# Kernel optimization log

Hardware: AMD Instinct MI355X
Metric: run time of the kernel (lower is better)

Reference implementation:

```python
import jax, jax.numpy as jnp
import numpy as np
from math import ceil

N = 20000   # nodes
E = 320000  # edges
D = 128     # num_features == num_hidden
K = ceil(N * 0.1)  # 2000 PMA seeds


def _gcn(x, W, b, src, dst):
    # PyG GCNConv: add self-loops, symmetric deg^-1/2 normalization, sum-aggregate, bias
    n = x.shape[0]
    sl = jnp.arange(n)
    s = jnp.concatenate([src, sl])
    d = jnp.concatenate([dst, sl])
    deg = jax.ops.segment_sum(jnp.ones((s.shape[0],), x.dtype), d, num_segments=n)
    dinv = jax.lax.rsqrt(jnp.maximum(deg, 1e-12))
    norm = dinv[s] * dinv[d]
    h = x @ W
    return jax.ops.segment_sum(h[s] * norm[:, None], d, num_segments=n) + b


def _ln(x, g, b):
    m = jnp.mean(x, -1, keepdims=True)
    v = jnp.var(x, -1, keepdims=True)
    return (x - m) * jax.lax.rsqrt(v + 1e-5) * g + b


def setup_inputs() -> dict:
    key = jax.random.key(0)
    ks = jax.random.split(key, 32)
    w = lambda i, shape: jax.random.normal(ks[i], shape, jnp.float32) * 0.05
    z = lambda shape: jnp.zeros(shape, jnp.float32)
    o = lambda shape: jnp.ones(shape, jnp.float32)
    return {
        "x": jax.random.normal(ks[0], (N, D), jnp.float32),
        "edge_index": jax.random.randint(ks[1], (2, E), 0, N),
        "batch": jnp.zeros((N,), jnp.int32),
        "W1": w(2, (D, D)), "b1": z((D,)),
        "W2": w(3, (D, D)), "b2": z((D,)),
        "S": w(4, (1, K, D)),
        "Wq": w(5, (D, D)), "bq": z((D,)),
        "Wk": w(6, (D, D)), "bk": z((D,)),
        "Wv": w(7, (D, D)), "bv": z((D,)),
        "Wo": w(8, (D, D)), "bo": z((D,)),
        "g0": o((D,)), "be0": z((D,)),
        "g1": o((D,)), "be1": z((D,)),
        "Wl": w(9, (D, D)), "bl": z((D,)),
        "W3": w(10, (D, D)), "b3": z((D,)),
        "W4": w(11, (D, D)), "b4": z((D,)),
        "W5": w(12, (D, D)), "b5": z((D,)),
    }


def reference(x, edge_index, batch, W1, b1, W2, b2, S, Wq, bq, Wk, bk, Wv, bv,
              Wo, bo, g0, be0, g1, be1, Wl, bl, W3, b3, W4, b4, W5, b5):
    src, dst = edge_index[0], edge_index[1]
    h = jax.nn.relu(_gcn(x, W1, b1, src, dst))
    h = jax.nn.relu(_gcn(h, W2, b2, src, dst))
    # B=1 dense batch: mask all-true -> additive attention mask is 0
    Q = S @ Wq + bq                        # [1,K,D]
    Kd = _gcn(h, Wk, bk, src, dst)[None]   # [1,N,D]  (mab_conv='GCN')
    Vd = _gcn(h, Wv, bv, src, dst)[None]   # [1,N,D]
    score = jnp.einsum('bkd,bnd->bkn', Q, Kd) / jnp.sqrt(jnp.float32(D))
    A = jax.nn.softmax(score, axis=1)      # cluster=True: softmax over seed dim
    out = Q + jnp.einsum('bkn,bnd->bkd', A, Vd)
    out = _ln(out, g0, be0)
    out = out + jax.nn.relu(out @ Wo + bo)
    out = _ln(out, g1, be1)
    xl = out @ Wl + bl                     # [1,K,D]
    x_out = jnp.einsum('bkn,bkd->bnd', A, xl)[0]  # attn^T @ x -> [N,D], mask all-true
    h = jax.nn.relu(_gcn(x_out, W3, b3, src, dst))
    h = jax.nn.relu(_gcn(h, W4, b4, src, dst))
    return _gcn(h, W5, b5, src, dst)       # [N,D]
```

## Files before the change

### kernel.cpp

```cpp
#include <hip/hip_runtime.h>

#define NN 20000
#define EE 320000
#define KK 2000
#define KP 2048
#define SCALE 0.08838834764831845f
#define ZSPLIT 16
#define ACHUNKS 625

typedef const float* cfp;
typedef __attribute__((ext_vector_type(8))) short sh8;
typedef __attribute__((ext_vector_type(4))) float f32x4;

static __device__ __forceinline__ float4 ld4(const float* p){ return *reinterpret_cast<const float4*>(p); }
static __device__ __forceinline__ void st4(float* p, float4 v){ *reinterpret_cast<float4*>(p) = v; }

static __device__ __forceinline__ unsigned short f2bf(float f){
    unsigned int u = __float_as_uint(f);
    u = (u + 0x7FFFu + ((u >> 16) & 1u)) >> 16;
    return (unsigned short)u;
}
static __device__ __forceinline__ float bf2f(unsigned short h){
    return __uint_as_float(((unsigned int)h) << 16);
}
static __device__ __forceinline__ sh8 lds8(const unsigned short* p){ return *reinterpret_cast<const sh8*>(p); }

__global__ __launch_bounds__(256) void k_count(const int* dst, int* deg){
    int i = blockIdx.x*256 + threadIdx.x;
    if (i < EE) atomicAdd(&deg[dst[i]], 1);
}

__global__ __launch_bounds__(256) void k_dinv(const int* deg, float* dinv){
    int n = blockIdx.x*256 + threadIdx.x;
    if (n < NN) dinv[n] = rsqrtf((float)deg[n] + 1.0f);
}

__global__ __launch_bounds__(1024) void k_scan(const int* cnt, int* rows){
    __shared__ int part[1024];
    int t = threadIdx.x;
    int base = t*20;
    int s = 0;
    for (int i = 0; i < 20; ++i){ int idx = base+i; if (idx < NN) s += cnt[idx]; }
    part[t] = s; __syncthreads();
    for (int off = 1; off < 1024; off <<= 1){
        int v = (t >= off) ? part[t-off] : 0;
        __syncthreads();
        part[t] += v;
        __syncthreads();
    }
    int run = part[t] - s;
    for (int i = 0; i < 20; ++i){
        int idx = base+i;
        if (idx < NN){ rows[idx] = run; run += cnt[idx]; }
    }
    if (t == 0) rows[NN] = EE;
}

__global__ __launch_bounds__(256) void k_fill(const int* src, const int* dst, const int* rows,
                                              int* cursor, int* col){
    int i = blockIdx.x*256 + threadIdx.x;
    if (i < EE){
        int d = dst[i];
        int pos = rows[d] + atomicAdd(&cursor[d], 1);
        col[pos] = src[i];
    }
}

__global__ __launch_bounds__(256) void conv_wT(cfp w0, cfp w1, cfp w2, cfp w3, cfp w4, cfp w5, cfp w6,
                                               unsigned short* wts){
    const float* in;
    switch (blockIdx.z){
        case 0: in = w0; break; case 1: in = w1; break; case 2: in = w2; break;
        case 3: in = w3; break; case 4: in = w4; break; case 5: in = w5; break;
        default: in = w6; break;
    }
    unsigned short* out = wts + (size_t)blockIdx.z*16384;
    __shared__ float t[64][65];
    int r0 = blockIdx.x*64, c0 = blockIdx.y*64;
    int tid = threadIdx.x;
    for (int i = tid; i < 64*16; i += 256){
        int r = i >> 4, c4 = (i & 15) * 4;
        float4 v = ld4(in + (size_t)(r0+r)*128 + c0 + c4);
        t[r][c4+0]=v.x; t[r][c4+1]=v.y; t[r][c4+2]=v.z; t[r][c4+3]=v.w;
    }
    __syncthreads();
    for (int i = tid; i < 64*16; i += 256){
        int c = i >> 4, r4 = (i & 15) * 4;
        ushort4 o;
        o.x = f2bf(t[r4+0][c]); o.y = f2bf(t[r4+1][c]);
        o.z = f2bf(t[r4+2][c]); o.w = f2bf(t[r4+3][c]);
        *reinterpret_cast<ushort4*>(out + (size_t)(c0+c)*128 + r0 + r4) = o;
    }
}

__global__ __launch_bounds__(512) void gemm128(const float* __restrict__ A, const float* __restrict__ Wm,
                                               float* __restrict__ C, int M,
                                               const float* bias, const float* resid, int relu){
    __shared__ __align__(16) float Ws[128*132];
    __shared__ float As[64*129];
    int tid = threadIdx.x;
    int r0 = blockIdx.x*64;
    for (int i = tid; i < 128*32; i += 512){
        int r = i >> 5, c4 = (i & 31) * 4;
        float4 v = ld4(Wm + r*128 + c4);
        st4(&Ws[r*132 + c4], v);
    }
    for (int i = tid; i < 64*32; i += 512){
        int r = i >> 5, c4 = (i & 31) * 4;
        float4 v = (r0 + r < M) ? ld4(A + (size_t)(r0+r)*128 + c4) : make_float4(0,0,0,0);
        As[r*129 + c4+0] = v.x; As[r*129 + c4+1] = v.y;
        As[r*129 + c4+2] = v.z; As[r*129 + c4+3] = v.w;
    }
    __syncthreads();
    int a = tid >> 5;
    int b = tid & 31;
    float acc[4][4] = {};
    #pragma unroll 4
    for (int d = 0; d < 128; ++d){
        float4 w = ld4(&Ws[d*132 + 4*b]);
        float wv[4] = {w.x, w.y, w.z, w.w};
        float av[4];
        #pragma unroll
        for (int i = 0; i < 4; ++i) av[i] = As[(4*a+i)*129 + d];
        #pragma unroll
        for (int i = 0; i < 4; ++i)
            #pragma unroll
            for (int j = 0; j < 4; ++j)
                acc[i][j] += av[i]*wv[j];
    }
    int cc = 4*b;
    #pragma unroll
    for (int i = 0; i < 4; ++i){
        int r = r0 + 4*a + i;
        if (r < M){
            float v[4];
            #pragma unroll
            for (int j = 0; j < 4; ++j) v[j] = acc[i][j];
            if (bias){
                #pragma unroll
                for (int j = 0; j < 4; ++j) v[j] += bias[cc+j];
            }
            if (relu){
                #pragma unroll
                for (int j = 0; j < 4; ++j) v[j] = fmaxf(v[j], 0.f);
            }
            if (resid){
                float4 rv = ld4(resid + (size_t)r*128 + cc);
                v[0]+=rv.x; v[1]+=rv.y; v[2]+=rv.z; v[3]+=rv.w;
            }
            st4(C + (size_t)r*128 + cc, make_float4(v[0],v[1],v[2],v[3]));
        }
    }
}

__global__ __launch_bounds__(256) void tgemm(const unsigned short* __restrict__ A, int M,
                                             const unsigned short* __restrict__ Wt,
                                             const float* __restrict__ rscale,
                                             unsigned short* __restrict__ C){
    int tid = threadIdx.x;
    int wave = tid >> 6, lane = tid & 63;
    int wm = wave >> 1, wn = wave & 1;
    int m_base = blockIdx.x*64 + wm*32;
    int n_base = blockIdx.y*64 + wn*32;
    int l15 = lane & 15;
    int roff = (lane >> 4) * 8;
    const unsigned short* ap0 = A + (size_t)(m_base + l15)*128 + roff;
    const unsigned short* ap1 = ap0 + 16*128;
    const unsigned short* b0p = Wt + (size_t)(n_base + l15)*128 + roff;
    const unsigned short* b1p = b0p + 16*128;
    f32x4 acc00 = (f32x4)0.f, acc01 = (f32x4)0.f, acc10 = (f32x4)0.f, acc11 = (f32x4)0.f;
    #pragma unroll
    for (int r = 0; r < 128; r += 32){
        sh8 a0 = lds8(ap0 + r);
        sh8 a1 = lds8(ap1 + r);
        sh8 b0 = lds8(b0p + r);
        sh8 b1 = lds8(b1p + r);
        acc00 = __builtin_amdgcn_mfma_f32_16x16x32_bf16(a0, b0, acc00, 0, 0, 0);
        acc01 = __builtin_amdgcn_mfma_f32_16x16x32_bf16(a0, b1, acc01, 0, 0, 0);
        acc10 = __builtin_amdgcn_mfma_f32_16x16x32_bf16(a1, b0, acc10, 0, 0, 0);
        acc11 = __builtin_amdgcn_mfma_f32_16x16x32_bf16(a1, b1, acc11, 0, 0, 0);
    }
    int rq = (lane >> 4) * 4;
    f32x4 accs[2][2] = {{acc00, acc01},{acc10, acc11}};
    #pragma unroll
    for (int mi = 0; mi < 2; ++mi){
        #pragma unroll
        for (int ni = 0; ni < 2; ++ni){
            f32x4 a = accs[mi][ni];
            int gn = n_base + ni*16 + l15;
            #pragma unroll
            for (int reg = 0; reg < 4; ++reg){
                int gm = m_base + mi*16 + rq + reg;
                if (gm < M) C[(size_t)gm*128 + gn] = f2bf(a[reg] * (rscale ? rscale[gm] : 1.f));
            }
        }
    }
}

__global__ __launch_bounds__(256) void gcn_agg_bf(const unsigned short* __restrict__ y, const float* __restrict__ dinv,
                                                  const int* __restrict__ rows, const int* __restrict__ col,
                                                  const float* __restrict__ bias, void* __restrict__ outv,
                                                  int relu, int out_fp32){
    int wid = (int)((blockIdx.x*256 + threadIdx.x) >> 6);
    int lane = threadIdx.x & 63;
    if (wid >= NN) return;
    int f = lane*2;
    ushort2 u = *reinterpret_cast<const ushort2*>(y + (size_t)wid*128 + f);
    float ax = bf2f(u.x), ay = bf2f(u.y);
    int s = rows[wid], e = rows[wid+1];
    int j = s;
    int e8 = s + ((e - s) & ~7);
    for (; j < e8; j += 8){
        ushort2 v[8];
        #pragma unroll
        for (int q = 0; q < 8; ++q){
            int c = col[j+q];
            v[q] = *reinterpret_cast<const ushort2*>(y + (size_t)c*128 + f);
        }
        #pragma unroll
        for (int q = 0; q < 8; ++q){ ax += bf2f(v[q].x); ay += bf2f(v[q].y); }
    }
    for (; j < e; ++j){
        int c0 = col[j];
        ushort2 v0 = *reinterpret_cast<const ushort2*>(y + (size_t)c0*128 + f);
        ax += bf2f(v0.x); ay += bf2f(v0.y);
    }
    float dn = dinv[wid];
    float ox = ax*dn + bias[f];
    float oy = ay*dn + bias[f+1];
    if (relu){ ox = fmaxf(ox, 0.f); oy = fmaxf(oy, 0.f); }
    if (out_fp32){
        *reinterpret_cast<float2*>((float*)outv + (size_t)wid*128 + f) = make_float2(ox, oy);
    } else {
        ushort2 o; o.x = f2bf(ox); o.y = f2bf(oy);
        *reinterpret_cast<ushort2*>((unsigned short*)outv + (size_t)wid*128 + f) = o;
    }
}

__global__ __launch_bounds__(256) void conv_bf16(const float* __restrict__ in, unsigned short* __restrict__ out, int n4){
    int i = blockIdx.x*256 + threadIdx.x;
    if (i < n4){
        float4 v = ld4(in + (size_t)i*4);
        ushort4 o;
        o.x = f2bf(v.x); o.y = f2bf(v.y); o.z = f2bf(v.z); o.w = f2bf(v.w);
        *reinterpret_cast<ushort4*>(out + (size_t)i*4) = o;
    }
}

__global__ __launch_bounds__(256) void conv_bf16_T(const float* __restrict__ in, unsigned short* __restrict__ out,
                                                   int M, int ldout, const float* __restrict__ rscale){
    __shared__ float t[64][65];
    int r0 = blockIdx.x*64, c0 = blockIdx.y*64;
    int tid = threadIdx.x;
    for (int i = tid; i < 64*16; i += 256){
        int r = i >> 4, c4 = (i & 15) * 4;
        float4 v = (r0 + r < M) ? ld4(in + (size_t)(r0+r)*128 + c0 + c4) : make_float4(0,0,0,0);
        if (rscale && r0 + r < M){
            float sc = rscale[r0 + r];
            v.x *= sc; v.y *= sc; v.z *= sc; v.w *= sc;
        }
        t[r][c4+0]=v.x; t[r][c4+1]=v.y; t[r][c4+2]=v.z; t[r][c4+3]=v.w;
    }
    __syncthreads();
    for (int i = tid; i < 64*16; i += 256){
        int c = i >> 4, r4 = (i & 15) * 4;
        if (r0 + r4 < M){
            ushort4 o;
            o.x = f2bf(t[r4+0][c]); o.y = f2bf(t[r4+1][c]);
            o.z = f2bf(t[r4+2][c]); o.w = f2bf(t[r4+3][c]);
            *reinterpret_cast<ushort4*>(out + (size_t)(c0+c)*ldout + r0 + r4) = o;
        }
    }
}

__global__ __launch_bounds__(256) void k_rcp32(const float* __restrict__ zp, const float* __restrict__ dinv,
                                               float* __restrict__ zinv, float* __restrict__ zdinv){
    int n = blockIdx.x*256 + threadIdx.x;
    if (n < NN){
        float s = 0.f;
        #pragma unroll
        for (int y = 0; y < 32; ++y) s += zp[(size_t)y*NN + n];
        float zi = 1.f / s;
        zinv[n] = zi;
        zdinv[n] = zi * dinv[n];
    }
}

__global__ __launch_bounds__(256) void s_gemm_exp(const unsigned short* __restrict__ Kb,
                                                  const unsigned short* __restrict__ Qb2,
                                                  unsigned short* __restrict__ E, float* __restrict__ zpart){
    __shared__ unsigned short Es[64*68];
    int tid = threadIdx.x;
    int wave = tid >> 6, lane = tid & 63;
    int wm = wave >> 1, wn = wave & 1;
    int n_blk = blockIdx.x*64, k_blk = blockIdx.y*64;
    int l15 = lane & 15;
    int roff = (lane >> 4) * 8;
    const unsigned short* ap0 = Kb + (size_t)(n_blk + wm*32 + l15)*128 + roff;
    const unsigned short* ap1 = ap0 + 16*128;
    const unsigned short* bp0 = Qb2 + (size_t)(k_blk + wn*32 + l15)*128 + roff;
    const unsigned short* bp1 = bp0 + 16*128;
    f32x4 acc00 = (f32x4)0.f, acc01 = (f32x4)0.f, acc10 = (f32x4)0.f, acc11 = (f32x4)0.f;
    #pragma unroll
    for (int r = 0; r < 128; r += 32){
        sh8 a0 = lds8(ap0 + r);
        sh8 a1 = lds8(ap1 + r);
        sh8 b0 = lds8(bp0 + r);
        sh8 b1 = lds8(bp1 + r);
        acc00 = __builtin_amdgcn_mfma_f32_16x16x32_bf16(a0, b0, acc00, 0, 0, 0);
        acc01 = __builtin_amdgcn_mfma_f32_16x16x32_bf16(a0, b1, acc01, 0, 0, 0);
        acc10 = __builtin_amdgcn_mfma_f32_16x16x32_bf16(a1, b0, acc10, 0, 0, 0);
        acc11 = __builtin_amdgcn_mfma_f32_16x16x32_bf16(a1, b1, acc11, 0, 0, 0);
    }
    int rq = (lane >> 4) * 4;
    f32x4 accs[2][2] = {{acc00, acc01},{acc10, acc11}};
    #pragma unroll
    for (int mi = 0; mi < 2; ++mi){
        #pragma unroll
        for (int ni = 0; ni < 2; ++ni){
            f32x4 a = accs[mi][ni];
            int c_loc = wn*32 + ni*16 + l15;
            bool kv = (k_blk + c_loc) < KK;
            #pragma unroll
            for (int reg = 0; reg < 4; ++reg){
                int r_loc = wm*32 + mi*16 + rq + reg;
                float e = kv ? __expf(a[reg]*SCALE) : 0.f;
                Es[r_loc*68 + c_loc] = f2bf(e);
            }
        }
    }
    __syncthreads();
    if (tid < 64){
        int n = n_blk + tid;
        if (n < NN){
            float s = 0.f;
            #pragma unroll 8
            for (int j = 0; j < 64; ++j) s += bf2f(Es[tid*68 + j]);
            zpart[(size_t)blockIdx.y*NN + n] = s;
        }
    }
    for (int i = tid; i < 512; i += 256){
        int r = i >> 3, c8 = (i & 7) * 8;
        if (n_blk + r < NN){
            ushort4 lo = *reinterpret_cast<const ushort4*>(&Es[r*68 + c8]);
            ushort4 hi = *reinterpret_cast<const ushort4*>(&Es[r*68 + c8 + 4]);
            unsigned short* dst = E + (size_t)(n_blk + r)*KP + k_blk + c8;
            *reinterpret_cast<ushort4*>(dst) = lo;
            *reinterpret_cast<ushort4*>(dst + 4) = hi;
        }
    }
}

__global__ __launch_bounds__(256) void attn_gemm(const unsigned short* __restrict__ E,
                                                 const unsigned short* __restrict__ Vt,
                                                 float* __restrict__ part){
    __shared__ unsigned short As[64*36];
    int tid = threadIdx.x;
    int wave = tid >> 6, lane = tid & 63;
    int kk0 = blockIdx.x*64;
    int per = (ACHUNKS + ZSPLIT - 1) / ZSPLIT;
    int c0 = blockIdx.y*per;
    int c1 = min(ACHUNKS, c0 + per);
    int l15 = lane & 15;
    int q8 = (lane >> 4) * 8;
    int d0 = wave*32;
    int n_l = tid & 31;
    int k8 = (tid >> 5) * 8;
    f32x4 acc[4][2];
    #pragma unroll
    for (int g = 0; g < 4; ++g){ acc[g][0] = (f32x4)0.f; acc[g][1] = (f32x4)0.f; }
    const unsigned short* ebase = E + (size_t)n_l*KP + kk0 + k8;
    const unsigned short* vb0p = Vt + (size_t)(d0 + l15)*NN + q8;
    const unsigned short* vb1p = vb0p + (size_t)16*NN;
    sh8 etmp = lds8(ebase + (size_t)c0*32*KP);
    sh8 vb0 = lds8(vb0p + c0*32);
    sh8 vb1 = lds8(vb1p + c0*32);
    for (int ch = c0; ch < c1; ++ch){
        unsigned short tmp[8];
        *reinterpret_cast<sh8*>(tmp) = etmp;
        #pragma unroll
        for (int j = 0; j < 8; ++j) As[(k8 + j)*36 + n_l] = tmp[j];
        __syncthreads();
        sh8 etn = (sh8)0, vbn0 = (sh8)0, vbn1 = (sh8)0;
        if (ch + 1 < c1){
            etn  = lds8(ebase + (size_t)(ch+1)*32*KP);
            vbn0 = lds8(vb0p + (ch+1)*32);
            vbn1 = lds8(vb1p + (ch+1)*32);
        }
        #pragma unroll
        for (int g = 0; g < 4; ++g){
            const unsigned short* ap = &As[(g*16 + l15)*36 + q8];
            union { struct { ushort4 lo, hi; } u; sh8 v; } af;
            af.u.lo = *reinterpret_cast<const ushort4*>(ap);
            af.u.hi = *reinterpret_cast<const ushort4*>(ap + 4);
            acc[g][0] = __builtin_amdgcn_mfma_f32_16x16x32_bf16(af.v, vb0, acc[g][0], 0, 0, 0);
            acc[g][1] = __builtin_amdgcn_mfma_f32_16x16x32_bf16(af.v, vb1, acc[g][1], 0, 0, 0);
        }
        __syncthreads();
        etmp = etn; vb0 = vbn0; vb1 = vbn1;
    }
    float* pbase = part + (size_t)blockIdx.y*KK*128;
    int rq = (lane >> 4) * 4;
    #pragma unroll
    for (int g = 0; g < 4; ++g){
        #pragma unroll
        for (int ni = 0; ni < 2; ++ni){
            int d = d0 + ni*16 + l15;
            #pragma unroll
            for (int reg = 0; reg < 4; ++reg){
                int kk = kk0 + g*16 + rq + reg;
                if (kk < KK) pbase[(size_t)kk*128 + d] = acc[g][ni][reg];
            }
        }
    }
}

__global__ __launch_bounds__(256) void xout_gemm(const unsigned short* __restrict__ E,
                                                 const unsigned short* __restrict__ B,
                                                 float* __restrict__ xpart){
    int tid = threadIdx.x;
    int wave = tid >> 6, lane = tid & 63;
    int wm = wave >> 1, wn = wave & 1;
    int m_base = blockIdx.x*64 + wm*32;
    int n_base = blockIdx.y*64 + wn*32;
    int kz = blockIdx.z*1024;
    int l15 = lane & 15;
    int roff = (lane >> 4) * 8;
    const unsigned short* ap0 = E + (size_t)(m_base + l15)*KP + kz + roff;
    const unsigned short* ap1 = ap0 + (size_t)16*KP;
    const unsigned short* bp0 = B + (size_t)(n_base + l15)*KP + kz + roff;
    const unsigned short* bp1 = bp0 + (size_t)16*KP;
    f32x4 acc00 = (f32x4)0.f, acc01 = (f32x4)0.f, acc10 = (f32x4)0.f, acc11 = (f32x4)0.f;
    sh8 a0 = lds8(ap0),      a1 = lds8(ap1),      a2 = lds8(ap0 + 32), a3 = lds8(ap1 + 32);
    sh8 b0 = lds8(bp0),      b1 = lds8(bp1),      b2 = lds8(bp0 + 32), b3 = lds8(bp1 + 32);
    for (int r = 0; r < 1024; r += 64){
        int rn = r + 64;
        sh8 na0 = (sh8)0, na1 = (sh8)0, na2 = (sh8)0, na3 = (sh8)0;
        sh8 nb0 = (sh8)0, nb1 = (sh8)0, nb2 = (sh8)0, nb3 = (sh8)0;
        if (rn < 1024){
            na0 = lds8(ap0 + rn);      na1 = lds8(ap1 + rn);
            na2 = lds8(ap0 + rn + 32); na3 = lds8(ap1 + rn + 32);
            nb0 = lds8(bp0 + rn);      nb1 = lds8(bp1 + rn);
            nb2 = lds8(bp0 + rn + 32); nb3 = lds8(bp1 + rn + 32);
        }
        acc00 = __builtin_amdgcn_mfma_f32_16x16x32_bf16(a0, b0, acc00, 0, 0, 0);
        acc01 = __builtin_amdgcn_mfma_f32_16x16x32_bf16(a0, b1, acc01, 0, 0, 0);
        acc10 = __builtin_amdgcn_mfma_f32_16x16x32_bf16(a1, b0, acc10, 0, 0, 0);
        acc11 = __builtin_amdgcn_mfma_f32_16x16x32_bf16(a1, b1, acc11, 0, 0, 0);
        acc00 = __builtin_amdgcn_mfma_f32_16x16x32_bf16(a2, b2, acc00, 0, 0, 0);
        acc01 = __builtin_amdgcn_mfma_f32_16x16x32_bf16(a2, b3, acc01, 0, 0, 0);
        acc10 = __builtin_amdgcn_mfma_f32_16x16x32_bf16(a3, b2, acc10, 0, 0, 0);
        acc11 = __builtin_amdgcn_mfma_f32_16x16x32_bf16(a3, b3, acc11, 0, 0, 0);
        a0 = na0; a1 = na1; a2 = na2; a3 = na3;
        b0 = nb0; b1 = nb1; b2 = nb2; b3 = nb3;
    }
    float* pbase = xpart + (size_t)blockIdx.z*NN*128;
    int rq = (lane >> 4) * 4;
    f32x4 accs[2][2] = {{acc00, acc01},{acc10, acc11}};
    #pragma unroll
    for (int mi = 0; mi < 2; ++mi){
        #pragma unroll
        for (int ni = 0; ni < 2; ++ni){
            f32x4 a = accs[mi][ni];
            int gn = n_base + ni*16 + l15;
            #pragma unroll
            for (int reg = 0; reg < 4; ++reg){
                int gm = m_base + mi*16 + rq + reg;
                if (gm < NN) pbase[(size_t)gm*128 + gn] = a[reg];
            }
        }
    }
}

__global__ __launch_bounds__(256) void xred(const float* __restrict__ xp, const float* __restrict__ zdinv,
                                            unsigned short* __restrict__ out){
    int i = blockIdx.x*256 + threadIdx.x;
    if (i < NN*32){
        int row = i >> 5;
        float4 p0 = ld4(xp + (size_t)i*4);
        float4 p1 = ld4(xp + (size_t)NN*128 + (size_t)i*4);
        float sc = zdinv[row];
        ushort4 o;
        o.x = f2bf((p0.x + p1.x)*sc);
        o.y = f2bf((p0.y + p1.y)*sc);
        o.z = f2bf((p0.z + p1.z)*sc);
        o.w = f2bf((p0.w + p1.w)*sc);
        *reinterpret_cast<ushort4*>(out + (size_t)i*4) = o;
    }
}

__global__ __launch_bounds__(128) void ln_ker(const float* __restrict__ in, int nparts,
                                              const float* __restrict__ resid,
                                              const float* __restrict__ g, const float* __restrict__ be,
                                              float* __restrict__ out){
    __shared__ float rs[128], rq[128];
    int r = blockIdx.x, t = threadIdx.x;
    float v = 0.f;
    for (int p = 0; p < nparts; ++p) v += in[(size_t)p*KK*128 + r*128 + t];
    if (resid) v += resid[r*128 + t];
    rs[t] = v; rq[t] = v*v;
    __syncthreads();
    for (int off = 64; off > 0; off >>= 1){
        if (t < off){ rs[t] += rs[t+off]; rq[t] += rq[t+off]; }
        __syncthreads();
    }
    float mean = rs[0]*(1.f/128.f);
    float var = rq[0]*(1.f/128.f) - mean*mean;
    out[r*128 + t] = (v - mean)*rsqrtf(var + 1e-5f)*g[t] + be[t];
}

extern "C" void kernel_launch(void* const* d_in, const int* in_sizes, int n_in,
                              void* d_out, int out_size, void* d_ws, size_t ws_size,
                              hipStream_t stream){
    cfp x  = (cfp)d_in[0];
    const int* ei = (const int*)d_in[1];
    const int* esrc = ei;
    const int* edst = ei + EE;
    cfp W1=(cfp)d_in[3], b1=(cfp)d_in[4], W2=(cfp)d_in[5], b2=(cfp)d_in[6];
    cfp S =(cfp)d_in[7];
    cfp Wq=(cfp)d_in[8],  bq=(cfp)d_in[9],  Wk=(cfp)d_in[10], bk=(cfp)d_in[11];
    cfp Wv=(cfp)d_in[12], bv=(cfp)d_in[13], Wo=(cfp)d_in[14], bo=(cfp)d_in[15];
    cfp g0=(cfp)d_in[16], be0=(cfp)d_in[17], g1=(cfp)d_in[18], be1=(cfp)d_in[19];
    cfp Wl=(cfp)d_in[20], bl=(cfp)d_in[21], W3=(cfp)d_in[22], b3=(cfp)d_in[23];
    cfp W4=(cfp)d_in[24], b4=(cfp)d_in[25], W5=(cfp)d_in[26], b5=(cfp)d_in[27];

    char* wsb = (char*)d_ws;
    const size_t MB = 1048576;
    int*   deg    = (int*)  (wsb + 0);
    float* dinv   = (float*)(wsb + 81920);
    int*   rows   = (int*)  (wsb + 163840);
    int*   cursor = (int*)  (wsb + 245760);
    int*   col    = (int*)  (wsb + 327680);
    float* Qb     = (float*)(wsb + 2*MB);
    float* o1     = (float*)(wsb + 3*MB);
    float* o2     = (float*)(wsb + 4*MB);
    float* o3     = (float*)(wsb + 5*MB);
    float* xlb    = (float*)(wsb + 6*MB);
    float* zpart  = (float*)(wsb + 7*MB);
    float* zinv   = (float*)(wsb + 10*MB);
    float* zdinv  = (float*)(wsb + 10*MB + 131072);
    unsigned short* Wts  = (unsigned short*)(wsb + 10*MB + 262144);
    unsigned short* Qbf  = (unsigned short*)(wsb + 11*MB);
    unsigned short* xlt3 = (unsigned short*)(wsb + 11*MB + 524288);
    unsigned short* xbf = (unsigned short*)(wsb + 12*MB);
    unsigned short* h1  = (unsigned short*)(wsb + 17*MB);
    unsigned short* h2  = (unsigned short*)(wsb + 22*MB);
    unsigned short* ybuf= (unsigned short*)(wsb + 27*MB);
    unsigned short* Kbf = (unsigned short*)(wsb + 32*MB);
    unsigned short* Vtz = (unsigned short*)(wsb + 37*MB);
    float* NB3    = (float*)(wsb + 42*MB);
    float* part   = (float*)(wsb + 42*MB);
    float* xpart  = (float*)(wsb + 42*MB);
    unsigned short* E = (unsigned short*)(wsb + 62*MB);
    float* outp   = (float*)d_out;
    unsigned short* h3 = xbf;
    unsigned short* h4 = h1;

    (void)hipMemsetAsync(deg, 0, NN*sizeof(int), stream);
    (void)hipMemsetAsync(cursor, 0, NN*sizeof(int), stream);
    (void)hipMemsetAsync(xlt3, 0, 128*KP*sizeof(unsigned short), stream);

    k_count<<<1250, 256, 0, stream>>>(edst, deg);
    k_dinv<<<79, 256, 0, stream>>>(deg, dinv);
    k_scan<<<1, 1024, 0, stream>>>(deg, rows);
    k_fill<<<1250, 256, 0, stream>>>(esrc, edst, rows, cursor, col);

    conv_wT<<<dim3(2,2,7), 256, 0, stream>>>(W1, W2, Wk, Wv, W3, W4, W5, Wts);
    conv_bf16<<<2500, 256, 0, stream>>>(x, xbf, NN*32);
    unsigned short* W1t = Wts;
    unsigned short* W2t = Wts + 16384;
    unsigned short* Wkt = Wts + 2*16384;
    unsigned short* Wvt = Wts + 3*16384;
    unsigned short* W4t = Wts + 5*16384;
    unsigned short* W5t = Wts + 6*16384;

    const int GN = 313;
    const int GK = 32;

    tgemm<<<dim3(GN,2), 256, 0, stream>>>(xbf, NN, W1t, dinv, ybuf);
    gcn_agg_bf<<<5000, 256, 0, stream>>>(ybuf, dinv, rows, col, b1, h1, 1, 0);
    tgemm<<<dim3(GN,2), 256, 0, stream>>>(h1, NN, W2t, dinv, ybuf);
    gcn_agg_bf<<<5000, 256, 0, stream>>>(ybuf, dinv, rows, col, b2, h2, 1, 0);
    tgemm<<<dim3(GN,2), 256, 0, stream>>>(h2, NN, Wkt, dinv, ybuf);
    gcn_agg_bf<<<5000, 256, 0, stream>>>(ybuf, dinv, rows, col, bk, Kbf, 0, 0);
    gemm128<<<GK, 512, 0, stream>>>(S, Wq, Qb, KK, bq, nullptr, 0);
    conv_bf16<<<250, 256, 0, stream>>>(Qb, Qbf, KK*32);
    s_gemm_exp<<<dim3(GN, GK), 256, 0, stream>>>(Kbf, Qbf, E, zpart);
    k_rcp32<<<79, 256, 0, stream>>>(zpart, dinv, zinv, zdinv);
    tgemm<<<dim3(GN,2), 256, 0, stream>>>(h2, NN, Wvt, dinv, ybuf);
    gcn_agg_bf<<<5000, 256, 0, stream>>>(ybuf, dinv, rows, col, bv, NB3, 0, 1);
    conv_bf16_T<<<dim3(GN, 2), 256, 0, stream>>>(NB3, Vtz, NN, NN, zinv);
    attn_gemm<<<dim3(GK, ZSPLIT), 256, 0, stream>>>(E, Vtz, part);
    ln_ker<<<KK, 128, 0, stream>>>(part, ZSPLIT, Qb, g0, be0, o1);
    gemm128<<<GK, 512, 0, stream>>>(o1, Wo, o2, KK, bo, o1, 1);
    ln_ker<<<KK, 128, 0, stream>>>(o2, 1, nullptr, g1, be1, o3);
    gemm128<<<GK, 512, 0, stream>>>(o3, Wl, xlb, KK, bl, nullptr, 0);
    gemm128<<<GK, 512, 0, stream>>>(xlb, W3, o1, KK, nullptr, nullptr, 0);
    conv_bf16_T<<<dim3(GK, 2), 256, 0, stream>>>(o1, xlt3, KK, KP, nullptr);
    xout_gemm<<<dim3(GN, 2, 2), 256, 0, stream>>>(E, xlt3, xpart);
    xred<<<2500, 256, 0, stream>>>(xpart, zdinv, ybuf);
    gcn_agg_bf<<<5000, 256, 0, stream>>>(ybuf, dinv, rows, col, b3, h3, 1, 0);
    tgemm<<<dim3(GN,2), 256, 0, stream>>>(h3, NN, W4t, dinv, ybuf);
    gcn_agg_bf<<<5000, 256, 0, stream>>>(ybuf, dinv, rows, col, b4, h4, 1, 0);
    tgemm<<<dim3(GN,2), 256, 0, stream>>>(h4, NN, W5t, dinv, ybuf);
    gcn_agg_bf<<<5000, 256, 0, stream>>>(ybuf, dinv, rows, col, b5, outp, 0, 1);
}
```

Measured before the change: 637.4 us.

## Reuse K tiles across seed blocks in score-exp and widen xout tile to full D

s_gemm_exp now has each block keep its 64-row K tile in registers and loop over 8 seed sub-blocks of 64, prefetching the next Q tile. The row sums are accumulated in fp32 registers and reduced with shuffles rather than summed back from the bf16 values in shared memory. The grid drops from 32 to 4 seed chunks, and k_rcp32 sums 4 partials instead of 32. xout_gemm now computes all 128 output columns per block with 8 accumulators per wave, so each block reads its E rows once instead of twice. The cost is fewer blocks, more registers and extra barriers per block.

```diff
diff --git a/kernel.cpp b/kernel.cpp
--- a/kernel.cpp
+++ b/kernel.cpp
@@ -7,6 +7,7 @@
 #define SCALE 0.08838834764831845f
 #define ZSPLIT 16
 #define ACHUNKS 625
+#define ZCH 4
 
 typedef const float* cfp;
 typedef __attribute__((ext_vector_type(8))) short sh8;
@@ -279,7 +280,7 @@
     if (n < NN){
         float s = 0.f;
         #pragma unroll
-        for (int y = 0; y < 32; ++y) s += zp[(size_t)y*NN + n];
+        for (int y = 0; y < ZCH; ++y) s += zp[(size_t)y*NN + n];
         float zi = 1.f / s;
         zinv[n] = zi;
         zdinv[n] = zi * dinv[n];
@@ -290,64 +291,99 @@
                                                   const unsigned short* __restrict__ Qb2,
                                                   unsigned short* __restrict__ E, float* __restrict__ zpart){
     __shared__ unsigned short Es[64*68];
+    __shared__ float zsh[2][64];
     int tid = threadIdx.x;
     int wave = tid >> 6, lane = tid & 63;
     int wm = wave >> 1, wn = wave & 1;
-    int n_blk = blockIdx.x*64, k_blk = blockIdx.y*64;
+    int n_blk = blockIdx.x*64;
+    int k_base = blockIdx.y*512;
     int l15 = lane & 15;
     int roff = (lane >> 4) * 8;
+    int rq = (lane >> 4) * 4;
     const unsigned short* ap0 = Kb + (size_t)(n_blk + wm*32 + l15)*128 + roff;
     const unsigned short* ap1 = ap0 + 16*128;
-    const unsigned short* bp0 = Qb2 + (size_t)(k_blk + wn*32 + l15)*128 + roff;
-    const unsigned short* bp1 = bp0 + 16*128;
-    f32x4 acc00 = (f32x4)0.f, acc01 = (f32x4)0.f, acc10 = (f32x4)0.f, acc11 = (f32x4)0.f;
-    #pragma unroll
-    for (int r = 0; r < 128; r += 32){
-        sh8 a0 = lds8(ap0 + r);
-        sh8 a1 = lds8(ap1 + r);
-        sh8 b0 = lds8(bp0 + r);
-        sh8 b1 = lds8(bp1 + r);
-        acc00 = __builtin_amdgcn_mfma_f32_16x16x32_bf16(a0, b0, acc00, 0, 0, 0);
-        acc01 = __builtin_amdgcn_mfma_f32_16x16x32_bf16(a0, b1, acc01, 0, 0, 0);
-        acc10 = __builtin_amdgcn_mfma_f32_16x16x32_bf16(a1, b0, acc10, 0, 0, 0);
-        acc11 = __builtin_amdgcn_mfma_f32_16x16x32_bf16(a1, b1, acc11, 0, 0, 0);
-    }
-    int rq = (lane >> 4) * 4;
-    f32x4 accs[2][2] = {{acc00, acc01},{acc10, acc11}};
+    sh8 a0[4], a1[4];
+    #pragma unroll
+    for (int r = 0; r < 4; ++r){ a0[r] = lds8(ap0 + r*32); a1[r] = lds8(ap1 + r*32); }
+    const unsigned short* qbase = Qb2 + (size_t)(k_base + wn*32 + l15)*128 + roff;
+    sh8 q0[4], q1[4];
+    #pragma unroll
+    for (int r = 0; r < 4; ++r){ q0[r] = lds8(qbase + r*32); q1[r] = lds8(qbase + 16*128 + r*32); }
+    float zacc[2][4] = {{0.f,0.f,0.f,0.f},{0.f,0.f,0.f,0.f}};
+    for (int kb = 0; kb < 8; ++kb){
+        sh8 n0[4], n1[4];
+        if (kb < 7){
+            const unsigned short* qn = qbase + (size_t)(kb+1)*64*128;
+            #pragma unroll
+            for (int r = 0; r < 4; ++r){ n0[r] = lds8(qn + r*32); n1[r] = lds8(qn + 16*128 + r*32); }
+        } else {
+            #pragma unroll
+            for (int r = 0; r < 4; ++r){ n0[r] = (sh8)0; n1[r] = (sh8)0; }
+        }
+        f32x4 acc00 = (f32x4)0.f, acc01 = (f32x4)0.f, acc10 = (f32x4)0.f, acc11 = (f32x4)0.f;
+        #pragma unroll
+        for (int r = 0; r < 4; ++r){
+            acc00 = __builtin_amdgcn_mfma_f32_16x16x32_bf16(a0[r], q0[r], acc00, 0, 0, 0);
+            acc01 = __builtin_amdgcn_mfma_f32_16x16x32_bf16(a0[r], q1[r], acc01, 0, 0, 0);
+            acc10 = __builtin_amdgcn_mfma_f32_16x16x32_bf16(a1[r], q0[r], acc10, 0, 0, 0);
+            acc11 = __builtin_amdgcn_mfma_f32_16x16x32_bf16(a1[r], q1[r], acc11, 0, 0, 0);
+        }
+        __syncthreads();
+        int kcol = k_base + kb*64;
+        f32x4 accs[2][2] = {{acc00, acc01},{acc10, acc11}};
+        #pragma unroll
+        for (int mi = 0; mi < 2; ++mi){
+            #pragma unroll
+            for (int ni = 0; ni < 2; ++ni){
+                f32x4 a = accs[mi][ni];
+                int c_loc = wn*32 + ni*16 + l15;
+                bool kv = (kcol + c_loc) < KK;
+                #pragma unroll
+                for (int reg = 0; reg < 4; ++reg){
+                    float e = kv ? __expf(a[reg]*SCALE) : 0.f;
+                    Es[(wm*32 + mi*16 + rq + reg)*68 + c_loc] = f2bf(e);
+                    zacc[mi][reg] += e;
+                }
+            }
+        }
+        __syncthreads();
+        for (int i = tid; i < 512; i += 256){
+            int r = i >> 3, c8 = (i & 7) * 8;
+            if (n_blk + r < NN){
+                ushort4 lo = *reinterpret_cast<const ushort4*>(&Es[r*68 + c8]);
+                ushort4 hi = *reinterpret_cast<const ushort4*>(&Es[r*68 + c8 + 4]);
+                unsigned short* dst = E + (size_t)(n_blk + r)*KP + kcol + c8;
+                *reinterpret_cast<ushort4*>(dst) = lo;
+                *reinterpret_cast<ushort4*>(dst + 4) = hi;
+            }
+        }
+        #pragma unroll
+        for (int r = 0; r < 4; ++r){ q0[r] = n0[r]; q1[r] = n1[r]; }
+    }
     #pragma unroll
     for (int mi = 0; mi < 2; ++mi){
         #pragma unroll
-        for (int ni = 0; ni < 2; ++ni){
-            f32x4 a = accs[mi][ni];
-            int c_loc = wn*32 + ni*16 + l15;
-            bool kv = (k_blk + c_loc) < KK;
-            #pragma unroll
-            for (int reg = 0; reg < 4; ++reg){
-                int r_loc = wm*32 + mi*16 + rq + reg;
-                float e = kv ? __expf(a[reg]*SCALE) : 0.f;
-                Es[r_loc*68 + c_loc] = f2bf(e);
-            }
-        }
+        for (int reg = 0; reg < 4; ++reg){
+            float v = zacc[mi][reg];
+            v += __shfl_xor(v, 1);
+            v += __shfl_xor(v, 2);
+            v += __shfl_xor(v, 4);
+            v += __shfl_xor(v, 8);
+            zacc[mi][reg] = v;
+        }
+    }
+    if (l15 == 0){
+        int h = lane >> 4;
+        #pragma unroll
+        for (int mi = 0; mi < 2; ++mi)
+            #pragma unroll
+            for (int reg = 0; reg < 4; ++reg)
+                zsh[wn][wm*32 + mi*16 + h*4 + reg] = zacc[mi][reg];
     }
     __syncthreads();
     if (tid < 64){
         int n = n_blk + tid;
-        if (n < NN){
-            float s = 0.f;
-            #pragma unroll 8
-            for (int j = 0; j < 64; ++j) s += bf2f(Es[tid*68 + j]);
-            zpart[(size_t)blockIdx.y*NN + n] = s;
-        }
-    }
-    for (int i = tid; i < 512; i += 256){
-        int r = i >> 3, c8 = (i & 7) * 8;
-        if (n_blk + r < NN){
-            ushort4 lo = *reinterpret_cast<const ushort4*>(&Es[r*68 + c8]);
-            ushort4 hi = *reinterpret_cast<const ushort4*>(&Es[r*68 + c8 + 4]);
-            unsigned short* dst = E + (size_t)(n_blk + r)*KP + k_blk + c8;
-            *reinterpret_cast<ushort4*>(dst) = lo;
-            *reinterpret_cast<ushort4*>(dst + 4) = hi;
-        }
+        if (n < NN) zpart[(size_t)blockIdx.y*NN + n] = zsh[0][tid] + zsh[1][tid];
     }
 }
 
@@ -422,51 +458,68 @@
     int wave = tid >> 6, lane = tid & 63;
     int wm = wave >> 1, wn = wave & 1;
     int m_base = blockIdx.x*64 + wm*32;
-    int n_base = blockIdx.y*64 + wn*32;
-    int kz = blockIdx.z*1024;
+    int kz = blockIdx.y*1024;
     int l15 = lane & 15;
     int roff = (lane >> 4) * 8;
+    int rq = (lane >> 4) * 4;
     const unsigned short* ap0 = E + (size_t)(m_base + l15)*KP + kz + roff;
     const unsigned short* ap1 = ap0 + (size_t)16*KP;
-    const unsigned short* bp0 = B + (size_t)(n_base + l15)*KP + kz + roff;
+    const unsigned short* bp0 = B + (size_t)(wn*32 + l15)*KP + kz + roff;
     const unsigned short* bp1 = bp0 + (size_t)16*KP;
-    f32x4 acc00 = (f32x4)0.f, acc01 = (f32x4)0.f, acc10 = (f32x4)0.f, acc11 = (f32x4)0.f;
-    sh8 a0 = lds8(ap0),      a1 = lds8(ap1),      a2 = lds8(ap0 + 32), a3 = lds8(ap1 + 32);
-    sh8 b0 = lds8(bp0),      b1 = lds8(bp1),      b2 = lds8(bp0 + 32), b3 = lds8(bp1 + 32);
+    const unsigned short* bp2 = bp0 + (size_t)64*KP;
+    const unsigned short* bp3 = bp0 + (size_t)80*KP;
+    f32x4 acc[2][4];
+    #pragma unroll
+    for (int mi = 0; mi < 2; ++mi)
+        #pragma unroll
+        for (int dt = 0; dt < 4; ++dt) acc[mi][dt] = (f32x4)0.f;
+    sh8 a_[2][2], b_[4][2];
+    a_[0][0]=lds8(ap0);    a_[0][1]=lds8(ap0+32);
+    a_[1][0]=lds8(ap1);    a_[1][1]=lds8(ap1+32);
+    b_[0][0]=lds8(bp0);    b_[0][1]=lds8(bp0+32);
+    b_[1][0]=lds8(bp1);    b_[1][1]=lds8(bp1+32);
+    b_[2][0]=lds8(bp2);    b_[2][1]=lds8(bp2+32);
+    b_[3][0]=lds8(bp3);    b_[3][1]=lds8(bp3+32);
     for (int r = 0; r < 1024; r += 64){
         int rn = r + 64;
-        sh8 na0 = (sh8)0, na1 = (sh8)0, na2 = (sh8)0, na3 = (sh8)0;
-        sh8 nb0 = (sh8)0, nb1 = (sh8)0, nb2 = (sh8)0, nb3 = (sh8)0;
+        sh8 na[2][2], nb[4][2];
         if (rn < 1024){
-            na0 = lds8(ap0 + rn);      na1 = lds8(ap1 + rn);
-            na2 = lds8(ap0 + rn + 32); na3 = lds8(ap1 + rn + 32);
-            nb0 = lds8(bp0 + rn);      nb1 = lds8(bp1 + rn);
-            nb2 = lds8(bp0 + rn + 32); nb3 = lds8(bp1 + rn + 32);
-        }
-        acc00 = __builtin_amdgcn_mfma_f32_16x16x32_bf16(a0, b0, acc00, 0, 0, 0);
-        acc01 = __builtin_amdgcn_mfma_f32_16x16x32_bf16(a0, b1, acc01, 0, 0, 0);
-        acc10 = __builtin_amdgcn_mfma_f32_16x16x32_bf16(a1, b0, acc10, 0, 0, 0);
-        acc11 = __builtin_amdgcn_mfma_f32_16x16x32_bf16(a1, b1, acc11, 0, 0, 0);
-        acc00 = __builtin_amdgcn_mfma_f32_16x16x32_bf16(a2, b2, acc00, 0, 0, 0);
-        acc01 = __builtin_amdgcn_mfma_f32_16x16x32_bf16(a2, b3, acc01, 0, 0, 0);
-        acc10 = __builtin_amdgcn_mfma_f32_16x16x32_bf16(a3, b2, acc10, 0, 0, 0);
-        acc11 = __builtin_amdgcn_mfma_f32_16x16x32_bf16(a3, b3, acc11, 0, 0, 0);
-        a0 = na0; a1 = na1; a2 = na2; a3 = na3;
-        b0 = nb0; b1 = nb1; b2 = nb2; b3 = nb3;
-    }
-    float* pbase = xpart + (size_t)blockIdx.z*NN*128;
-    int rq = (lane >> 4) * 4;
-    f32x4 accs[2][2] = {{acc00, acc01},{acc10, acc11}};
+            na[0][0]=lds8(ap0+rn);    na[0][1]=lds8(ap0+rn+32);
+            na[1][0]=lds8(ap1+rn);    na[1][1]=lds8(ap1+rn+32);
+            nb[0][0]=lds8(bp0+rn);    nb[0][1]=lds8(bp0+rn+32);
+            nb[1][0]=lds8(bp1+rn);    nb[1][1]=lds8(bp1+rn+32);
+            nb[2][0]=lds8(bp2+rn);    nb[2][1]=lds8(bp2+rn+32);
+            nb[3][0]=lds8(bp3+rn);    nb[3][1]=lds8(bp3+rn+32);
+        } else {
+            #pragma unroll
+            for (int mi = 0; mi < 2; ++mi){ na[mi][0] = (sh8)0; na[mi][1] = (sh8)0; }
+            #pragma unroll
+            for (int dt = 0; dt < 4; ++dt){ nb[dt][0] = (sh8)0; nb[dt][1] = (sh8)0; }
+        }
+        #pragma unroll
+        for (int h = 0; h < 2; ++h){
+            #pragma unroll
+            for (int mi = 0; mi < 2; ++mi)
+                #pragma unroll
+                for (int dt = 0; dt < 4; ++dt)
+                    acc[mi][dt] = __builtin_amdgcn_mfma_f32_16x16x32_bf16(a_[mi][h], b_[dt][h], acc[mi][dt], 0, 0, 0);
+        }
+        #pragma unroll
+        for (int mi = 0; mi < 2; ++mi){ a_[mi][0] = na[mi][0]; a_[mi][1] = na[mi][1]; }
+        #pragma unroll
+        for (int dt = 0; dt < 4; ++dt){ b_[dt][0] = nb[dt][0]; b_[dt][1] = nb[dt][1]; }
+    }
+    float* pbase = xpart + (size_t)blockIdx.y*NN*128;
     #pragma unroll
     for (int mi = 0; mi < 2; ++mi){
         #pragma unroll
-        for (int ni = 0; ni < 2; ++ni){
-            f32x4 a = accs[mi][ni];
-            int gn = n_base + ni*16 + l15;
+        for (int dt = 0; dt < 4; ++dt){
+            f32x4 a = acc[mi][dt];
+            int d = (dt >> 1)*64 + wn*32 + (dt & 1)*16 + l15;
             #pragma unroll
             for (int reg = 0; reg < 4; ++reg){
                 int gm = m_base + mi*16 + rq + reg;
-                if (gm < NN) pbase[(size_t)gm*128 + gn] = a[reg];
+                if (gm < NN) pbase[(size_t)gm*128 + d] = a[reg];
             }
         }
     }
@@ -585,7 +638,7 @@
     gcn_agg_bf<<<5000, 256, 0, stream>>>(ybuf, dinv, rows, col, bk, Kbf, 0, 0);
     gemm128<<<GK, 512, 0, stream>>>(S, Wq, Qb, KK, bq, nullptr, 0);
     conv_bf16<<<250, 256, 0, stream>>>(Qb, Qbf, KK*32);
-    s_gemm_exp<<<dim3(GN, GK), 256, 0, stream>>>(Kbf, Qbf, E, zpart);
+    s_gemm_exp<<<dim3(GN, ZCH), 256, 0, stream>>>(Kbf, Qbf, E, zpart);
     k_rcp32<<<79, 256, 0, stream>>>(zpart, dinv, zinv, zdinv);
     tgemm<<<dim3(GN,2), 256, 0, stream>>>(h2, NN, Wvt, dinv, ybuf);
     gcn_agg_bf<<<5000, 256, 0, stream>>>(ybuf, dinv, rows, col, bv, NB3, 0, 1);
@@ -597,7 +650,7 @@
     gemm128<<<GK, 512, 0, stream>>>(o3, Wl, xlb, KK, bl, nullptr, 0);
     gemm128<<<GK, 512, 0, stream>>>(xlb, W3, o1, KK, nullptr, nullptr, 0);
     conv_bf16_T<<<dim3(GK, 2), 256, 0, stream>>>(o1, xlt3, KK, KP, nullptr);
-    xout_gemm<<<dim3(GN, 2, 2), 256, 0, stream>>>(E, xlt3, xpart);
+    xout_gemm<<<dim3(GN, 2), 256, 0, stream>>>(E, xlt3, xpart);
     xred<<<2500, 256, 0, stream>>>(xpart, zdinv, ybuf);
     gcn_agg_bf<<<5000, 256, 0, stream>>>(ybuf, dinv, rows, col, b3, h3, 1, 0);
     tgemm<<<dim3(GN,2), 256, 0, stream>>>(h3, NN, W4t, dinv, ybuf);
```

Measured after the change: 606.7 us. 1.05x faster.
